# Performance work log

Measured on AMD Instinct MI355X. Metric: run time of the kernel, lower is better.

The kernel has to match this reference:

```python
import jax, jax.numpy as jnp
import numpy as np

N, E = 50000, 800000
IN, HID, HEADS, OUT = 128, 64, 2, 32
SLOPE = 0.2  # PyG leaky_relu default


def gat_conv(x, edge_index, edge_attr, W, att_src, att_dst, W_edge, att_edge, bias,
             heads, out_ch, concat):
    n = x.shape[0]
    src, dst = edge_index[0], edge_index[1]
    # add_self_loops with fill_value='mean': self-loop attr = mean of incoming edge_attr
    ones = jnp.ones((src.shape[0],), x.dtype)
    deg = jax.ops.segment_sum(ones, dst, num_segments=n)
    loop_attr = jax.ops.segment_sum(edge_attr, dst, num_segments=n) / jnp.maximum(deg, 1.0)[:, None]
    ar = jnp.arange(n)
    src = jnp.concatenate([src, ar])
    dst = jnp.concatenate([dst, ar])
    ea = jnp.concatenate([edge_attr, loop_attr], axis=0)  # [E+N, 1]
    # linear projections
    h = (x @ W).reshape(n, heads, out_ch)                      # [N,H,C]
    a_src = jnp.sum(h * att_src, axis=-1)                      # [N,H]
    a_dst = jnp.sum(h * att_dst, axis=-1)                      # [N,H]
    e_emb = (ea @ W_edge).reshape(-1, heads, out_ch)           # [E+N,H,C]
    a_edge = jnp.sum(e_emb * att_edge, axis=-1)                # [E+N,H]
    alpha = jax.nn.leaky_relu(a_src[src] + a_dst[dst] + a_edge, SLOPE)
    # segment softmax over destination nodes
    amax = jax.ops.segment_max(alpha, dst, num_segments=n)
    amax = jnp.where(jnp.isfinite(amax), amax, 0.0)
    ex = jnp.exp(alpha - amax[dst])
    denom = jax.ops.segment_sum(ex, dst, num_segments=n)
    coef = ex / (denom[dst] + 1e-16)                           # [E+N,H]
    out = jax.ops.segment_sum(h[src] * coef[:, :, None], dst, num_segments=n)  # [N,H,C]
    out = out.reshape(n, heads * out_ch) if concat else out.mean(axis=1)
    return out + bias


def setup_inputs() -> dict:
    key = jax.random.key(0)
    ks = jax.random.split(key, 16)
    g = lambda k, shape, fan: (jax.random.normal(k, shape, jnp.float32) / np.float32(np.sqrt(fan)))
    x = jax.random.normal(ks[0], (N, IN), jnp.float32)
    edge_index = jax.random.randint(ks[1], (2, E), 0, N)
    edge_weight = jax.random.uniform(ks[2], (E, 1), jnp.float32)
    return dict(
        x=x, edge_index=edge_index, edge_weight=edge_weight,
        W1=g(ks[3], (IN, HEADS * HID), IN),
        att_src1=g(ks[4], (1, HEADS, HID), HID),
        att_dst1=g(ks[5], (1, HEADS, HID), HID),
        We1=g(ks[6], (1, HEADS * HID), 1),
        att_edge1=g(ks[7], (1, HEADS, HID), HID),
        b1=jnp.zeros((HEADS * HID,), jnp.float32),
        W2=g(ks[8], (HEADS * HID, OUT), HEADS * HID),
        att_src2=g(ks[9], (1, 1, OUT), OUT),
        att_dst2=g(ks[10], (1, 1, OUT), OUT),
        We2=g(ks[11], (1, OUT), 1),
        att_edge2=g(ks[12], (1, 1, OUT), OUT),
        b2=jnp.zeros((OUT,), jnp.float32),
    )


def reference(x, edge_index, edge_weight, W1, att_src1, att_dst1, We1, att_edge1, b1,
              W2, att_src2, att_dst2, We2, att_edge2, b2):
    h = gat_conv(x, edge_index, edge_weight, W1, att_src1, att_dst1, We1, att_edge1, b1,
                 HEADS, HID, True)
    h = jax.nn.elu(h)
    out = gat_conv(h, edge_index, edge_weight, W2, att_src2, att_dst2, We2, att_edge2, b2,
                   1, OUT, False)
    return out
```

## Files before the change

kernel.cpp:

```cpp
#include <hip/hip_runtime.h>
#include <hip/hip_bf16.h>
#include <hip/hip_fp16.h>
#include <cstddef>

#define NN 50000
#define EE 800000
#define SB  196

typedef _Float16 half4v __attribute__((ext_vector_type(4)));
typedef _Float16 half8v __attribute__((ext_vector_type(8)));
typedef float    f32x4  __attribute__((ext_vector_type(4)));

__global__ void zero_k(unsigned long long* __restrict__ p) {
    int i = blockIdx.x * blockDim.x + threadIdx.x;
    if (i < NN) p[i] = 0ULL;
}

__global__ void hist_k(const int* __restrict__ ei, const float* __restrict__ ew,
                       unsigned long long* __restrict__ packed, int* __restrict__ rank) {
    int e = blockIdx.x * blockDim.x + threadIdx.x;
    if (e >= EE) return;
    int dst = ei[EE + e];
    unsigned q = (unsigned)(ew[e] * 16777216.0f + 0.5f);
    unsigned long long old =
        atomicAdd(&packed[dst], (1ULL << 40) | (unsigned long long)q);
    rank[e] = (int)(old >> 40);
}

__global__ void loopdiv_k(const unsigned long long* __restrict__ packed,
                          int* __restrict__ deg, float* __restrict__ loopa,
                          int* __restrict__ bsum) {
    __shared__ int sm[256];
    int t = threadIdx.x, n = blockIdx.x * 256 + t;
    int d = 0;
    if (n < NN) {
        unsigned long long p = packed[n];
        d = (int)(p >> 40);
        float ls = (float)(p & ((1ULL << 40) - 1)) * (1.0f / 16777216.0f);
        deg[n] = d;
        loopa[n] = ls / fmaxf((float)d, 1.0f);
    }
    sm[t] = d;
    __syncthreads();
    for (int off = 128; off; off >>= 1) {
        if (t < off) sm[t] += sm[t + off];
        __syncthreads();
    }
    if (!t) bsum[blockIdx.x] = sm[0];
}

__global__ void scan_top_k(const int* __restrict__ bsum, int* __restrict__ boff) {
    __shared__ int sm[256];
    int t = threadIdx.x;
    int v = (t < SB) ? bsum[t] : 0;
    sm[t] = v;
    __syncthreads();
    for (int off = 1; off < 256; off <<= 1) {
        int a = (t >= off) ? sm[t - off] : 0;
        __syncthreads();
        sm[t] += a;
        __syncthreads();
    }
    boff[t] = sm[t] - v;
}

__global__ void scan_final_k(const int* __restrict__ deg, const int* __restrict__ boff,
                             int* __restrict__ rowptr) {
    __shared__ int sm[256];
    int t = threadIdx.x, i = blockIdx.x * 256 + t;
    int v = (i < NN) ? deg[i] : 0;
    sm[t] = v;
    __syncthreads();
    for (int off = 1; off < 256; off <<= 1) {
        int a = (t >= off) ? sm[t - off] : 0;
        __syncthreads();
        sm[t] += a;
        __syncthreads();
    }
    if (i < NN) rowptr[i] = boff[blockIdx.x] + sm[t] - v;
    if (i == NN - 1) rowptr[NN] = boff[blockIdx.x] + sm[t];
}

__global__ void scatter_k(const int* __restrict__ ei, const float* __restrict__ ew,
                          const int* __restrict__ rowptr, const int* __restrict__ rank,
                          int2* __restrict__ csr) {
    int e = blockIdx.x * blockDim.x + threadIdx.x;
    if (e >= EE) return;
    int src = ei[e];
    int dst = ei[EE + e];
    int pos = rowptr[dst] + rank[e];
    csr[pos] = make_int2(src, __float_as_int(ew[e]));
}

__global__ void consts_k(const float* __restrict__ We1, const float* __restrict__ attE1,
                         const float* __restrict__ We2, const float* __restrict__ attE2,
                         float* __restrict__ cE) {
    __shared__ float sm[128];
    int t = threadIdx.x;
    sm[t] = We1[t] * attE1[t];
    __syncthreads();
    for (int off = 32; off; off >>= 1) {
        if ((t & 63) < off) sm[t] += sm[t + off];
        __syncthreads();
    }
    if (t == 0)  cE[0] = sm[0];
    if (t == 64) cE[1] = sm[64];
    __syncthreads();
    sm[t] = (t < 32) ? We2[t] * attE2[t] : 0.0f;
    __syncthreads();
    for (int off = 16; off; off >>= 1) {
        if (t < off) sm[t] += sm[t + off];
        __syncthreads();
    }
    if (t == 0) cE[2] = sm[0];
}

__global__ __launch_bounds__(256) void gemm1_k(const float* __restrict__ x,
                                               const float* __restrict__ W,
                                               const float* __restrict__ attS,
                                               const float* __restrict__ attD,
                                               __half* __restrict__ h1,
                                               float* __restrict__ asrc,
                                               float* __restrict__ adst) {
    __shared__ __align__(16) _Float16 xs[64 * 136];
    int rowbase = blockIdx.x * 64;
    int t = threadIdx.x;
    int wid = t >> 6, lane = t & 63;
    #pragma unroll
    for (int i = 0; i < 8; i++) {
        int idx = t + i * 256;
        int r = idx >> 5;
        int c4 = idx & 31;
        float4 v = make_float4(0.f, 0.f, 0.f, 0.f);
        if (rowbase + r < NN) v = ((const float4*)x)[(size_t)(rowbase + r) * 32 + c4];
        half4v hv = { (_Float16)v.x, (_Float16)v.y, (_Float16)v.z, (_Float16)v.w };
        *(half4v*)&xs[r * 136 + c4 * 4] = hv;
    }
    half8v bf[2][4];
    #pragma unroll
    for (int nt = 0; nt < 2; nt++)
        #pragma unroll
        for (int kk = 0; kk < 4; kk++) {
            int kb = kk * 32 + ((lane >> 4) << 3);
            int c = (wid << 5) + (nt << 4) + (lane & 15);
            half8v f;
            #pragma unroll
            for (int j = 0; j < 8; j++) f[j] = (_Float16)W[(kb + j) * 128 + c];
            bf[nt][kk] = f;
        }
    __syncthreads();
    int ar = lane & 15;
    int ak = (lane >> 4) << 3;
    f32x4 acc[4][2] = {};
    #pragma unroll
    for (int kk = 0; kk < 4; kk++) {
        half8v a[4];
        #pragma unroll
        for (int mt = 0; mt < 4; mt++)
            a[mt] = *(const half8v*)&xs[(mt * 16 + ar) * 136 + kk * 32 + ak];
        #pragma unroll
        for (int mt = 0; mt < 4; mt++)
            #pragma unroll
            for (int nt = 0; nt < 2; nt++)
                acc[mt][nt] = __builtin_amdgcn_mfma_f32_16x16x32_f16(
                    a[mt], bf[nt][kk], acc[mt][nt], 0, 0, 0);
    }
    __syncthreads();
    int drb = (lane >> 4) << 2;
    int dc = (wid << 5) + (lane & 15);
    #pragma unroll
    for (int mt = 0; mt < 4; mt++)
        #pragma unroll
        for (int nt = 0; nt < 2; nt++)
            #pragma unroll
            for (int r = 0; r < 4; r++)
                xs[(mt * 16 + drb + r) * 136 + dc + nt * 16] = (_Float16)acc[mt][nt][r];
    __syncthreads();
    int row = t >> 2;
    int cg = t & 3;
    int grow = rowbase + row;
    float sv = 0.f, dv = 0.f;
    #pragma unroll
    for (int k = 0; k < 4; k++) {
        int c0 = cg * 32 + k * 8;
        half8v hv = *(const half8v*)&xs[row * 136 + c0];
        if (grow < NN) *(half8v*)((_Float16*)h1 + (size_t)grow * 128 + c0) = hv;
        #pragma unroll
        for (int j = 0; j < 8; j++) {
            float f = (float)hv[j];
            sv += f * attS[c0 + j];
            dv += f * attD[c0 + j];
        }
    }
    sv += __shfl_xor(sv, 1);
    dv += __shfl_xor(dv, 1);
    if ((cg & 1) == 0 && grow < NN) {
        asrc[grow * 2 + (cg >> 1)] = sv;
        adst[grow * 2 + (cg >> 1)] = dv;
    }
}

__global__ __launch_bounds__(256) void gemm2_k(const __half* __restrict__ z1,
                                               const float* __restrict__ W,
                                               const float* __restrict__ attS,
                                               const float* __restrict__ attD,
                                               __half* __restrict__ h2,
                                               float* __restrict__ asrc,
                                               float* __restrict__ adst) {
    __shared__ __align__(16) _Float16 xs[64 * 136];
    int rowbase = blockIdx.x * 64;
    int t = threadIdx.x;
    int wid = t >> 6, lane = t & 63;
    #pragma unroll
    for (int i = 0; i < 4; i++) {
        int idx = t + i * 256;
        int r = idx >> 4;
        int c16 = idx & 15;
        uint4 v = make_uint4(0, 0, 0, 0);
        if (rowbase + r < NN) v = ((const uint4*)z1)[(size_t)(rowbase + r) * 16 + c16];
        *(uint4*)&xs[r * 136 + c16 * 8] = v;
    }
    half8v bf[2][4];
    #pragma unroll
    for (int nt = 0; nt < 2; nt++)
        #pragma unroll
        for (int kk = 0; kk < 4; kk++) {
            int kb = kk * 32 + ((lane >> 4) << 3);
            int c = (nt << 4) + (lane & 15);
            half8v f;
            #pragma unroll
            for (int j = 0; j < 8; j++) f[j] = (_Float16)W[(kb + j) * 32 + c];
            bf[nt][kk] = f;
        }
    __syncthreads();
    int ar = lane & 15;
    int ak = (lane >> 4) << 3;
    f32x4 acc[2] = {};
    #pragma unroll
    for (int kk = 0; kk < 4; kk++) {
        half8v a = *(const half8v*)&xs[(wid * 16 + ar) * 136 + kk * 32 + ak];
        #pragma unroll
        for (int nt = 0; nt < 2; nt++)
            acc[nt] = __builtin_amdgcn_mfma_f32_16x16x32_f16(a, bf[nt][kk], acc[nt], 0, 0, 0);
    }
    __syncthreads();
    int drb = (lane >> 4) << 2;
    #pragma unroll
    for (int nt = 0; nt < 2; nt++)
        #pragma unroll
        for (int r = 0; r < 4; r++)
            xs[(wid * 16 + drb + r) * 40 + (nt << 4) + (lane & 15)] = (_Float16)acc[nt][r];
    __syncthreads();
    int row = t >> 2;
    int c8 = (t & 3) * 8;
    int grow = rowbase + row;
    half8v hv = *(const half8v*)&xs[row * 40 + c8];
    if (grow < NN) *(half8v*)((_Float16*)h2 + (size_t)grow * 32 + c8) = hv;
    float sv = 0.f, dv = 0.f;
    #pragma unroll
    for (int j = 0; j < 8; j++) {
        float f = (float)hv[j];
        sv += f * attS[c8 + j];
        dv += f * attD[c8 + j];
    }
    sv += __shfl_xor(sv, 1);
    dv += __shfl_xor(dv, 1);
    sv += __shfl_xor(sv, 2);
    dv += __shfl_xor(dv, 2);
    if ((t & 3) == 0 && grow < NN) { asrc[grow] = sv; adst[grow] = dv; }
}

__global__ __launch_bounds__(256) void agg1_k(const int* __restrict__ rowptr,
                       const int2* __restrict__ csr, const float* __restrict__ loopa,
                       const __half* __restrict__ h1, const float* __restrict__ asrc,
                       const float* __restrict__ adst, const float* __restrict__ cE,
                       const float* __restrict__ b1, __half* __restrict__ z1) {
    __shared__ int    ssrc[4][128];
    __shared__ float2 sxx[4][128];
    int wid = threadIdx.x >> 6;
    int n = (blockIdx.x * blockDim.x + threadIdx.x) >> 6;
    int lane = threadIdx.x & 63;
    if (n >= NN) return;
    int start = rowptr[n];
    int degn = rowptr[n + 1] - start;
    int total = degn + 1;
    float c0 = cE[0], c1 = cE[1];
    float ad0 = adst[n * 2], ad1 = adst[n * 2 + 1];
    float la = loopa[n];
    float s0 = 0.f, s1 = 0.f;
    for (int i = lane; i < total; i += 64) {
        int src; float w;
        if (i < degn) { int2 sw = csr[start + i]; src = sw.x; w = __int_as_float(sw.y); }
        else          { src = n;                  w = la; }
        float2 as = *(const float2*)&asrc[src * 2];
        float e0 = as.x + ad0 + w * c0; e0 = e0 > 0.f ? e0 : 0.2f * e0;
        float e1 = as.y + ad1 + w * c1; e1 = e1 > 0.f ? e1 : 0.2f * e1;
        float x0 = __expf(e0), x1 = __expf(e1);
        s0 += x0; s1 += x1;
        if (i < 128) { ssrc[wid][i] = src; sxx[wid][i] = make_float2(x0, x1); }
    }
    for (int off = 32; off; off >>= 1) {
        s0 += __shfl_xor(s0, off);
        s1 += __shfl_xor(s1, off);
    }
    float inv0 = 1.0f / (s0 + 1e-16f), inv1 = 1.0f / (s1 + 1e-16f);
    int hsel = lane >> 5;
    float invh = hsel ? inv1 : inv0;
    float acc0 = 0.f, acc1 = 0.f;
    int nst = min(total, 128);
    int j = 0;
    for (; j + 8 <= nst; j += 8) {
        float cf[8]; float2 f[8];
        #pragma unroll
        for (int u = 0; u < 8; u++) {
            int s2 = ssrc[wid][j + u];
            float2 xv = sxx[wid][j + u];
            cf[u] = (hsel ? xv.y : xv.x) * invh;
            f[u] = __half22float2(*(const __half2*)&h1[(size_t)s2 * 128 + 2 * lane]);
        }
        #pragma unroll
        for (int u = 0; u < 8; u++) { acc0 += cf[u] * f[u].x; acc1 += cf[u] * f[u].y; }
    }
    for (; j < nst; j++) {
        int s2 = ssrc[wid][j];
        float2 xv = sxx[wid][j];
        float coef = (hsel ? xv.y : xv.x) * invh;
        float2 f = __half22float2(*(const __half2*)&h1[(size_t)s2 * 128 + 2 * lane]);
        acc0 += coef * f.x;
        acc1 += coef * f.y;
    }
    for (int base = 128; base < total; base += 64) {
        int i = base + lane;
        float cc0 = 0.f, cc1 = 0.f; int src = n;
        if (i < total) {
            float w;
            if (i < degn) { int2 sw = csr[start + i]; src = sw.x; w = __int_as_float(sw.y); }
            else          { w = la; }
            float2 as = *(const float2*)&asrc[src * 2];
            float e0 = as.x + ad0 + w * c0; e0 = e0 > 0.f ? e0 : 0.2f * e0;
            float e1 = as.y + ad1 + w * c1; e1 = e1 > 0.f ? e1 : 0.2f * e1;
            cc0 = __expf(e0) * inv0;
            cc1 = __expf(e1) * inv1;
        }
        int cnt = min(64, total - base);
        for (int jj = 0; jj < cnt; jj++) {
            int   s2 = __shfl(src, jj);
            float k0 = __shfl(cc0, jj);
            float k1 = __shfl(cc1, jj);
            float coef = hsel ? k1 : k0;
            float2 f = __half22float2(*(const __half2*)&h1[(size_t)s2 * 128 + 2 * lane]);
            acc0 += coef * f.x;
            acc1 += coef * f.y;
        }
    }
    float o0 = acc0 + b1[2 * lane];
    float o1 = acc1 + b1[2 * lane + 1];
    o0 = o0 > 0.f ? o0 : expm1f(o0);
    o1 = o1 > 0.f ? o1 : expm1f(o1);
    __half2 oz = __floats2half2_rn(o0, o1);
    *(__half2*)&z1[(size_t)n * 128 + 2 * lane] = oz;
}

__global__ __launch_bounds__(256) void agg2_k(const int* __restrict__ rowptr,
                       const int2* __restrict__ csr, const float* __restrict__ loopa,
                       const __half* __restrict__ h2, const float* __restrict__ asrc,
                       const float* __restrict__ adst, const float* __restrict__ cE,
                       const float* __restrict__ b2, float* __restrict__ out) {
    __shared__ float2 stash[4][128];
    int wid = threadIdx.x >> 6;
    int n = (blockIdx.x * blockDim.x + threadIdx.x) >> 6;
    int lane = threadIdx.x & 63;
    if (n >= NN) return;
    int start = rowptr[n];
    int degn = rowptr[n + 1] - start;
    int total = degn + 1;
    float c2 = cE[2];
    float aD = adst[n];
    float la = loopa[n];
    float s = 0.f;
    for (int i = lane; i < total; i += 64) {
        int src; float w;
        if (i < degn) { int2 sw = csr[start + i]; src = sw.x; w = __int_as_float(sw.y); }
        else          { src = n;                  w = la; }
        float e = asrc[src] + aD + w * c2;
        e = e > 0.f ? e : 0.2f * e;
        float x = __expf(e);
        s += x;
        if (i < 128) stash[wid][i] = make_float2(__int_as_float(src), x);
    }
    for (int off = 32; off; off >>= 1) s += __shfl_xor(s, off);
    float inv = 1.0f / (s + 1e-16f);
    int c = lane & 31;
    int half = lane >> 5;
    float acc = 0.f;
    int nst = min(total, 128);
    int c0n = (nst + 1) >> 1;
    int jb = half ? c0n : 0;
    int je = half ? nst : c0n;
    int j = jb;
    for (; j + 4 <= je; j += 4) {
        float cf[4], hv[4];
        #pragma unroll
        for (int u = 0; u < 4; u++) {
            float2 st = stash[wid][j + u];
            cf[u] = st.y * inv;
            hv[u] = __half2float(h2[(size_t)__float_as_int(st.x) * 32 + c]);
        }
        #pragma unroll
        for (int u = 0; u < 4; u++) acc += cf[u] * hv[u];
    }
    for (; j < je; j++) {
        float2 st = stash[wid][j];
        acc += st.y * inv * __half2float(h2[(size_t)__float_as_int(st.x) * 32 + c]);
    }
    for (int base = 128; base < total; base += 64) {
        int i = base + lane;
        float cc = 0.f; int src = n;
        if (i < total) {
            float w;
            if (i < degn) { int2 sw = csr[start + i]; src = sw.x; w = __int_as_float(sw.y); }
            else          { w = la; }
            float e = asrc[src] + aD + w * c2;
            e = e > 0.f ? e : 0.2f * e;
            cc = __expf(e) * inv;
        }
        int cnt = min(64, total - base);
        int h0n = (cnt + 1) >> 1;
        for (int k = 0; k < h0n; k++) {
            int jj = half ? (h0n + k) : k;
            int   s2 = __shfl(src, jj);
            float coef = __shfl(cc, jj);
            acc += coef * __half2float(h2[(size_t)s2 * 32 + c]);
        }
    }
    acc += __shfl_xor(acc, 32);
    if (lane < 32) out[(size_t)n * 32 + c] = acc + b2[c];
}

extern "C" void kernel_launch(void* const* d_in, const int* in_sizes, int n_in,
                              void* d_out, int out_size, void* d_ws, size_t ws_size,
                              hipStream_t stream) {
    const float* x     = (const float*)d_in[0];
    const int*   ei    = (const int*)d_in[1];
    const float* ew    = (const float*)d_in[2];
    const float* W1    = (const float*)d_in[3];
    const float* attS1 = (const float*)d_in[4];
    const float* attD1 = (const float*)d_in[5];
    const float* We1   = (const float*)d_in[6];
    const float* attE1 = (const float*)d_in[7];
    const float* b1    = (const float*)d_in[8];
    const float* W2    = (const float*)d_in[9];
    const float* attS2 = (const float*)d_in[10];
    const float* attD2 = (const float*)d_in[11];
    const float* We2   = (const float*)d_in[12];
    const float* attE2 = (const float*)d_in[13];
    const float* b2    = (const float*)d_in[14];

    char* ws = (char*)d_ws;
    size_t off = 0;
    auto alloc = [&](size_t bytes) -> void* {
        void* p = ws + off;
        off = (off + bytes + 255) & ~(size_t)255;
        return p;
    };
    unsigned long long* packed = (unsigned long long*)alloc((size_t)NN * 8);
    int*    rank    = (int*)alloc((size_t)EE * 4);
    int*    deg     = (int*)alloc((size_t)NN * 4);
    float*  loopa   = (float*)alloc((size_t)NN * 4);
    int*    rowptr  = (int*)alloc((size_t)(NN + 1) * 4);
    int2*   csr     = (int2*)alloc((size_t)EE * 8);
    __half* h1b     = (__half*)alloc((size_t)NN * 128 * 2);
    __half* z1      = (__half*)alloc((size_t)NN * 128 * 2);
    __half* h2b     = (__half*)alloc((size_t)NN * 32 * 2);
    float*  asrc1   = (float*)alloc((size_t)NN * 2 * 4);
    float*  adst1   = (float*)alloc((size_t)NN * 2 * 4);
    float*  asrc2   = (float*)alloc((size_t)NN * 4);
    float*  adst2   = (float*)alloc((size_t)NN * 4);
    float*  cE      = (float*)alloc(4 * 4);
    int*    bsum    = (int*)alloc(256 * 4);
    int*    boff    = (int*)alloc(256 * 4);

    const int EB  = (EE + 255) / 256;
    const int NWB = (NN * 64 + 255) / 256;
    const int GB  = (NN + 63) / 64;

    zero_k<<<SB, 256, 0, stream>>>(packed);
    hist_k<<<EB, 256, 0, stream>>>(ei, ew, packed, rank);
    consts_k<<<1, 128, 0, stream>>>(We1, attE1, We2, attE2, cE);
    loopdiv_k<<<SB, 256, 0, stream>>>(packed, deg, loopa, bsum);
    scan_top_k<<<1, 256, 0, stream>>>(bsum, boff);
    scan_final_k<<<SB, 256, 0, stream>>>(deg, boff, rowptr);
    scatter_k<<<EB, 256, 0, stream>>>(ei, ew, rowptr, rank, csr);

    gemm1_k<<<GB, 256, 0, stream>>>(x, W1, attS1, attD1, h1b, asrc1, adst1);
    agg1_k<<<NWB, 256, 0, stream>>>(rowptr, csr, loopa, h1b, asrc1, adst1, cE, b1, z1);

    gemm2_k<<<GB, 256, 0, stream>>>(z1, W2, attS2, attD2, h2b, asrc2, adst2);
    agg2_k<<<NWB, 256, 0, stream>>>(rowptr, csr, loopa, h2b, asrc2, adst2, cE, b2, (float*)d_out);
}
```

Baseline: 160.4 us.

## Use packed fp16 FMA with pre-normalized half coefficients in GAT aggregation

Both aggregation kernels now pre-normalize softmax coefficients into packed half2 values stored with the source index in shared memory, padded to multiples of 8. The inner gather loops then use packed fp16 multiply-add with periodic fp32 folding instead of fp32 conversion and FMA. agg2 is also remapped so each wavefront processes 4 edges at once with 16 lanes per edge, each lane holding a half2 channel pair. This cuts per-edge ALU work and address arithmetic and raises memory-level parallelism in agg2, at the cost of reduced accumulation precision and a serial per-edge tail loop for high-degree nodes.

```diff
diff --git a/kernel.cpp b/kernel.cpp
--- a/kernel.cpp
+++ b/kernel.cpp
@@ -9,6 +9,7 @@
 
 typedef _Float16 half4v __attribute__((ext_vector_type(4)));
 typedef _Float16 half8v __attribute__((ext_vector_type(8)));
+typedef _Float16 h2v    __attribute__((ext_vector_type(2)));
 typedef float    f32x4  __attribute__((ext_vector_type(4)));
 
 __global__ void zero_k(unsigned long long* __restrict__ p) {
@@ -277,6 +278,7 @@
                        const float* __restrict__ b1, __half* __restrict__ z1) {
     __shared__ int    ssrc[4][128];
     __shared__ float2 sxx[4][128];
+    __shared__ int2   spk[4][136];
     int wid = threadIdx.x >> 6;
     int n = (blockIdx.x * blockDim.x + threadIdx.x) >> 6;
     int lane = threadIdx.x & 63;
@@ -304,30 +306,36 @@
         s1 += __shfl_xor(s1, off);
     }
     float inv0 = 1.0f / (s0 + 1e-16f), inv1 = 1.0f / (s1 + 1e-16f);
+    int nst = min(total, 128);
+    int nst8 = (nst + 7) & ~7;
+    for (int i = lane; i < nst8; i += 64) {
+        int2 pk;
+        if (i < nst) {
+            float2 xv = sxx[wid][i];
+            __half2 hh = __floats2half2_rn(xv.x * inv0, xv.y * inv1);
+            pk = make_int2(ssrc[wid][i], *(int*)&hh);
+        } else pk = make_int2(n, 0);
+        spk[wid][i] = pk;
+    }
     int hsel = lane >> 5;
-    float invh = hsel ? inv1 : inv0;
+    unsigned psel = hsel ? 0x03020302u : 0x01000100u;
+    unsigned loff = (unsigned)lane * 4u;
+    const char* h1b_ = (const char*)h1;
     float acc0 = 0.f, acc1 = 0.f;
-    int nst = min(total, 128);
-    int j = 0;
-    for (; j + 8 <= nst; j += 8) {
-        float cf[8]; float2 f[8];
+    for (int j = 0; j < nst8; j += 8) {
+        h2v pa = {}, pb = {};
         #pragma unroll
         for (int u = 0; u < 8; u++) {
-            int s2 = ssrc[wid][j + u];
-            float2 xv = sxx[wid][j + u];
-            cf[u] = (hsel ? xv.y : xv.x) * invh;
-            f[u] = __half22float2(*(const __half2*)&h1[(size_t)s2 * 128 + 2 * lane]);
-        }
-        #pragma unroll
-        for (int u = 0; u < 8; u++) { acc0 += cf[u] * f[u].x; acc1 += cf[u] * f[u].y; }
-    }
-    for (; j < nst; j++) {
-        int s2 = ssrc[wid][j];
-        float2 xv = sxx[wid][j];
-        float coef = (hsel ? xv.y : xv.x) * invh;
-        float2 f = __half22float2(*(const __half2*)&h1[(size_t)s2 * 128 + 2 * lane]);
-        acc0 += coef * f.x;
-        acc1 += coef * f.y;
+            int2 st = spk[wid][j + u];
+            unsigned cs = __builtin_amdgcn_perm(0u, (unsigned)st.y, psel);
+            unsigned hb = *(const unsigned*)(h1b_ + (((unsigned)st.x << 8) + loff));
+            h2v c; __builtin_memcpy(&c, &cs, 4);
+            h2v h; __builtin_memcpy(&h, &hb, 4);
+            if (u & 1) pb = c * h + pb;
+            else       pa = c * h + pa;
+        }
+        acc0 += (float)pa.x + (float)pb.x;
+        acc1 += (float)pa.y + (float)pb.y;
     }
     for (int base = 128; base < total; base += 64) {
         int i = base + lane;
@@ -336,9 +344,8 @@
             float w;
             if (i < degn) { int2 sw = csr[start + i]; src = sw.x; w = __int_as_float(sw.y); }
             else          { w = la; }
-            float2 as = *(const float2*)&asrc[src * 2];
-            float e0 = as.x + ad0 + w * c0; e0 = e0 > 0.f ? e0 : 0.2f * e0;
-            float e1 = as.y + ad1 + w * c1; e1 = e1 > 0.f ? e1 : 0.2f * e1;
+            float e0 = asrc[src * 2]     + ad0 + w * c0; e0 = e0 > 0.f ? e0 : 0.2f * e0;
+            float e1 = asrc[src * 2 + 1] + ad1 + w * c1; e1 = e1 > 0.f ? e1 : 0.2f * e1;
             cc0 = __expf(e0) * inv0;
             cc1 = __expf(e1) * inv1;
         }
@@ -363,10 +370,12 @@
 
 __global__ __launch_bounds__(256) void agg2_k(const int* __restrict__ rowptr,
                        const int2* __restrict__ csr, const float* __restrict__ loopa,
-                       const __half* __restrict__ h2, const float* __restrict__ asrc,
+                       const __half* __restrict__ hh2, const float* __restrict__ asrc,
                        const float* __restrict__ adst, const float* __restrict__ cE,
                        const float* __restrict__ b2, float* __restrict__ out) {
-    __shared__ float2 stash[4][128];
+    __shared__ float2 sxx[4][128];
+    __shared__ int    ssrc[4][128];
+    __shared__ int2   spk[4][136];
     int wid = threadIdx.x >> 6;
     int n = (blockIdx.x * blockDim.x + threadIdx.x) >> 6;
     int lane = threadIdx.x & 63;
@@ -386,55 +395,68 @@
         e = e > 0.f ? e : 0.2f * e;
         float x = __expf(e);
         s += x;
-        if (i < 128) stash[wid][i] = make_float2(__int_as_float(src), x);
+        if (i < 128) { ssrc[wid][i] = src; sxx[wid][i] = make_float2(x, 0.f); }
     }
     for (int off = 32; off; off >>= 1) s += __shfl_xor(s, off);
     float inv = 1.0f / (s + 1e-16f);
-    int c = lane & 31;
-    int half = lane >> 5;
-    float acc = 0.f;
     int nst = min(total, 128);
-    int c0n = (nst + 1) >> 1;
-    int jb = half ? c0n : 0;
-    int je = half ? nst : c0n;
-    int j = jb;
-    for (; j + 4 <= je; j += 4) {
-        float cf[4], hv[4];
-        #pragma unroll
-        for (int u = 0; u < 4; u++) {
-            float2 st = stash[wid][j + u];
-            cf[u] = st.y * inv;
-            hv[u] = __half2float(h2[(size_t)__float_as_int(st.x) * 32 + c]);
-        }
-        #pragma unroll
-        for (int u = 0; u < 4; u++) acc += cf[u] * hv[u];
-    }
-    for (; j < je; j++) {
-        float2 st = stash[wid][j];
-        acc += st.y * inv * __half2float(h2[(size_t)__float_as_int(st.x) * 32 + c]);
-    }
-    for (int base = 128; base < total; base += 64) {
-        int i = base + lane;
-        float cc = 0.f; int src = n;
-        if (i < total) {
-            float w;
-            if (i < degn) { int2 sw = csr[start + i]; src = sw.x; w = __int_as_float(sw.y); }
-            else          { w = la; }
-            float e = asrc[src] + aD + w * c2;
-            e = e > 0.f ? e : 0.2f * e;
-            cc = __expf(e) * inv;
-        }
-        int cnt = min(64, total - base);
-        int h0n = (cnt + 1) >> 1;
-        for (int k = 0; k < h0n; k++) {
-            int jj = half ? (h0n + k) : k;
-            int   s2 = __shfl(src, jj);
-            float coef = __shfl(cc, jj);
-            acc += coef * __half2float(h2[(size_t)s2 * 32 + c]);
-        }
-    }
-    acc += __shfl_xor(acc, 32);
-    if (lane < 32) out[(size_t)n * 32 + c] = acc + b2[c];
+    int nst8 = (nst + 7) & ~7;
+    for (int i = lane; i < nst8; i += 64) {
+        int2 pk;
+        if (i < nst) {
+            float cn = sxx[wid][i].x * inv;
+            __half2 hc = __floats2half2_rn(cn, cn);
+            pk = make_int2(ssrc[wid][i], *(int*)&hc);
+        } else pk = make_int2(n, 0);
+        spk[wid][i] = pk;
+    }
+    int g  = lane >> 4;
+    int cp = lane & 15;
+    const char* h2b_ = (const char*)hh2;
+    unsigned coff = (unsigned)cp * 4u;
+    float fa0 = 0.f, fa1 = 0.f;
+    h2v pa = {}, pb = {};
+    int fold = 0;
+    for (int j = 0; j < nst8; j += 8) {
+        int2 st0 = spk[wid][j + g];
+        int2 st1 = spk[wid][j + 4 + g];
+        unsigned hb0 = *(const unsigned*)(h2b_ + (((unsigned)st0.x << 6) + coff));
+        unsigned hb1 = *(const unsigned*)(h2b_ + (((unsigned)st1.x << 6) + coff));
+        h2v c0v; __builtin_memcpy(&c0v, &st0.y, 4);
+        h2v c1v; __builtin_memcpy(&c1v, &st1.y, 4);
+        h2v h0; __builtin_memcpy(&h0, &hb0, 4);
+        h2v h1v; __builtin_memcpy(&h1v, &hb1, 4);
+        pa = c0v * h0 + pa;
+        pb = c1v * h1v + pb;
+        if (++fold == 4) {
+            fa0 += (float)pa.x + (float)pb.x;
+            fa1 += (float)pa.y + (float)pb.y;
+            pa = {}; pb = {};
+            fold = 0;
+        }
+    }
+    fa0 += (float)pa.x + (float)pb.x;
+    fa1 += (float)pa.y + (float)pb.y;
+    for (int i = 128; i < total; i++) {
+        int src; float w;
+        if (i < degn) { int2 sw = csr[start + i]; src = sw.x; w = __int_as_float(sw.y); }
+        else          { src = n;                  w = la; }
+        float e = asrc[src] + aD + w * c2;
+        e = e > 0.f ? e : 0.2f * e;
+        float cc = __expf(e) * inv;
+        if (g == 0) {
+            unsigned hb = *(const unsigned*)(h2b_ + (((unsigned)src << 6) + coff));
+            h2v h; __builtin_memcpy(&h, &hb, 4);
+            fa0 += cc * (float)h.x;
+            fa1 += cc * (float)h.y;
+        }
+    }
+    fa0 += __shfl_xor(fa0, 16); fa1 += __shfl_xor(fa1, 16);
+    fa0 += __shfl_xor(fa0, 32); fa1 += __shfl_xor(fa1, 32);
+    if (lane < 16) {
+        float2 o = make_float2(fa0 + b2[2 * cp], fa1 + b2[2 * cp + 1]);
+        *(float2*)&out[(size_t)n * 32 + 2 * cp] = o;
+    }
 }
 
 extern "C" void kernel_launch(void* const* d_in, const int* in_sizes, int n_in,
```

Measured after the change: 154.9 us. -3.5%, faster.
